# Kernel tuning notes

Hardware: AMD Instinct MI355X
Metric: run time of the kernel (lower is better)

## Reference

```python
import jax, jax.numpy as jnp
import numpy as np

EPS = 1e-12  # matches torch F.normalize eps


def _l2_normalize(x, axis=-1):
    # torch.F.normalize: x / max(||x||, eps)
    n = jnp.sqrt(jnp.sum(x * x, axis=axis, keepdims=True))
    return x / jnp.maximum(n, EPS)


def setup_inputs() -> dict:
    N, n_classes, embed_dim = 32768, 1000, 1024
    key = jax.random.key(0)
    k_feat, k_lab, k_proto = jax.random.split(key, 3)

    features = jax.random.normal(k_feat, (N, embed_dim), dtype=jnp.float32)

    # one-hot float labels, as expected by `torch.matmul(labels, self.mean_class)`
    y = jax.random.randint(k_lab, (N,), 0, n_classes)
    labels = jax.nn.one_hot(y, n_classes, dtype=jnp.float32)

    # predefined prototypes: orthonormal rows (ortho_group.rvs equivalent via QR)
    g = jax.random.normal(k_proto, (embed_dim, embed_dim), dtype=jnp.float32)
    q, _ = jnp.linalg.qr(g)
    mean_class = q[:n_classes]  # [n_classes, embed_dim], orthonormal rows

    return {"features": features, "labels": labels, "mean_class": mean_class}


def reference(features, labels, mean_class):
    # features: [N, D]; labels: [N, C] one-hot; mean_class: [C, D]
    # (3-D feature mean-pooling branch not exercised: inputs are 2-D)
    proto_y = labels @ mean_class                 # [N, D]
    f = _l2_normalize(features, axis=1)
    p = _l2_normalize(proto_y, axis=1)
    # diag(f @ p.T) == rowwise dot product -> same math, O(N*D) not O(N^2*D)
    cos = jnp.einsum("nd,nd->n", f, p)            # [N]
    return jnp.mean(1.0 - cos)
```

## Files before the change

kernel.cpp:

```cpp
#include <hip/hip_runtime.h>

constexpr int N_CLASSES = 1000;
constexpr int EMBED     = 1024;
constexpr int ROWS_PER_BLOCK = 8;

typedef float floatx4 __attribute__((ext_vector_type(4)));

__global__ __launch_bounds__(256) void angular_fused_kernel(
    const float* __restrict__ features,
    const float* __restrict__ labels,
    const float* __restrict__ mean_class,
    float* __restrict__ partials,
    int n_rows)
{
    const int tid  = threadIdx.x;
    const int lane = tid & 63;
    const int wave = tid >> 6;
    const int row0 = blockIdx.x * ROWS_PER_BLOCK;

    __shared__ int   s_cls[ROWS_PER_BLOCK];
    __shared__ float s_red[4];

    if (tid < N_CLASSES / 4) {
        #pragma unroll
        for (int r = 0; r < ROWS_PER_BLOCK; ++r) {
            const int row = row0 + r;
            if (row < n_rows) {
                const floatx4* lrow = (const floatx4*)(labels + (size_t)row * N_CLASSES);
                floatx4 v = __builtin_nontemporal_load(lrow + tid);
                if (v.x != 0.f || v.y != 0.f || v.z != 0.f || v.w != 0.f) {
                    int c = 4 * tid;
                    if      (v.y != 0.f) c += 1;
                    else if (v.z != 0.f) c += 2;
                    else if (v.w != 0.f) c += 3;
                    s_cls[r] = c;
                }
            }
        }
    }

    const int rA = row0 + 2 * wave;
    const int rB = rA + 1;
    const bool okA = rA < n_rows, okB = rB < n_rows;

    const floatx4* fArow = (const floatx4*)(features + (size_t)(okA ? rA : 0) * EMBED);
    const floatx4* fBrow = (const floatx4*)(features + (size_t)(okB ? rB : 0) * EMBED);
    floatx4 a0 = __builtin_nontemporal_load(fArow + lane);
    floatx4 a1 = __builtin_nontemporal_load(fArow + lane + 64);
    floatx4 a2 = __builtin_nontemporal_load(fArow + lane + 128);
    floatx4 a3 = __builtin_nontemporal_load(fArow + lane + 192);
    floatx4 b0 = __builtin_nontemporal_load(fBrow + lane);
    floatx4 b1 = __builtin_nontemporal_load(fBrow + lane + 64);
    floatx4 b2 = __builtin_nontemporal_load(fBrow + lane + 128);
    floatx4 b3 = __builtin_nontemporal_load(fBrow + lane + 192);

    __syncthreads();

    const int clsA = okA ? s_cls[2 * wave] : 0;
    const int clsB = okB ? s_cls[2 * wave + 1] : 0;
    const floatx4* pArow = (const floatx4*)(mean_class + (size_t)clsA * EMBED);
    const floatx4* pBrow = (const floatx4*)(mean_class + (size_t)clsB * EMBED);
    floatx4 pa0 = pArow[lane];
    floatx4 pa1 = pArow[lane + 64];
    floatx4 pa2 = pArow[lane + 128];
    floatx4 pa3 = pArow[lane + 192];
    floatx4 pb0 = pBrow[lane];
    floatx4 pb1 = pBrow[lane + 64];
    floatx4 pb2 = pBrow[lane + 128];
    floatx4 pb3 = pBrow[lane + 192];

    float ffA = 0.f, ppA = 0.f, fpA = 0.f;
    float ffB = 0.f, ppB = 0.f, fpB = 0.f;
    #define DOT3(FF, PP, FP, F, P) \
        FF += F.x*F.x + F.y*F.y + F.z*F.z + F.w*F.w; \
        PP += P.x*P.x + P.y*P.y + P.z*P.z + P.w*P.w; \
        FP += F.x*P.x + F.y*P.y + F.z*P.z + F.w*P.w;
    DOT3(ffA, ppA, fpA, a0, pa0) DOT3(ffA, ppA, fpA, a1, pa1)
    DOT3(ffA, ppA, fpA, a2, pa2) DOT3(ffA, ppA, fpA, a3, pa3)
    DOT3(ffB, ppB, fpB, b0, pb0) DOT3(ffB, ppB, fpB, b1, pb1)
    DOT3(ffB, ppB, fpB, b2, pb2) DOT3(ffB, ppB, fpB, b3, pb3)
    #undef DOT3

    #pragma unroll
    for (int msk = 1; msk < 64; msk <<= 1) {
        ffA += __shfl_xor(ffA, msk, 64);
        ppA += __shfl_xor(ppA, msk, 64);
        fpA += __shfl_xor(fpA, msk, 64);
        ffB += __shfl_xor(ffB, msk, 64);
        ppB += __shfl_xor(ppB, msk, 64);
        fpB += __shfl_xor(fpB, msk, 64);
    }

    float res = 0.f;
    if (okA) res += 1.0f - fpA / (fmaxf(sqrtf(ffA), 1e-12f) * fmaxf(sqrtf(ppA), 1e-12f));
    if (okB) res += 1.0f - fpB / (fmaxf(sqrtf(ffB), 1e-12f) * fmaxf(sqrtf(ppB), 1e-12f));

    if (lane == 0) s_red[wave] = res;
    __syncthreads();
    if (tid == 0)
        partials[blockIdx.x] = s_red[0] + s_red[1] + s_red[2] + s_red[3];
}

__global__ __launch_bounds__(256) void reduce_partials_kernel(
    const float* __restrict__ partials, int num_partials,
    float* __restrict__ out, float inv_n)
{
    const int tid  = threadIdx.x;
    const int lane = tid & 63;
    const int wave = tid >> 6;
    __shared__ float s_red[4];

    float acc = 0.0f;
    for (int i = tid; i < num_partials; i += 256)
        acc += partials[i];
    #pragma unroll
    for (int msk = 1; msk < 64; msk <<= 1)
        acc += __shfl_xor(acc, msk, 64);
    if (lane == 0) s_red[wave] = acc;
    __syncthreads();
    if (tid == 0)
        out[0] = (s_red[0] + s_red[1] + s_red[2] + s_red[3]) * inv_n;
}

extern "C" void kernel_launch(void* const* d_in, const int* in_sizes, int n_in,
                              void* d_out, int out_size, void* d_ws, size_t ws_size,
                              hipStream_t stream) {
    const float* features   = (const float*)d_in[0];
    const float* labels     = (const float*)d_in[1];
    const float* mean_class = (const float*)d_in[2];
    float* out = (float*)d_out;
    float* partials = (float*)d_ws;

    const int n_rows = in_sizes[0] / EMBED;
    const int num_blocks = (n_rows + ROWS_PER_BLOCK - 1) / ROWS_PER_BLOCK;

    angular_fused_kernel<<<num_blocks, 256, 0, stream>>>(
        features, labels, mean_class, partials, n_rows);
    reduce_partials_kernel<<<1, 256, 0, stream>>>(
        partials, num_blocks, out, 1.0f / (float)n_rows);
}
```

Measured before the change: 258.3 us.

## Stage one-hot label rows into LDS via async global_load_lds and scan per wave

Label rows are no longer scanned directly from global memory by 250 threads. Each wave now issues asynchronous global-to-LDS copies of its two label rows, and these overlap with the feature loads. After the barrier each wave scans its rows in LDS, then uses ballot and shuffle to pick the hot class index, made wave-uniform with readfirstlane. The nontemporal hints on the feature loads are also dropped. The aim is better memory-level parallelism on the dominant label traffic, at the cost of 32KB of LDS per block, which may reduce occupancy.

```diff
diff --git a/kernel.cpp b/kernel.cpp
--- a/kernel.cpp
+++ b/kernel.cpp
@@ -1,10 +1,19 @@
 #include <hip/hip_runtime.h>
+#include <stdint.h>
 
 constexpr int N_CLASSES = 1000;
 constexpr int EMBED     = 1024;
 constexpr int ROWS_PER_BLOCK = 8;
+constexpr int LAB_BYTES = N_CLASSES * 4;
 
 typedef float floatx4 __attribute__((ext_vector_type(4)));
+
+__device__ __forceinline__ void gl2lds16(const void* g, void* l) {
+    __builtin_amdgcn_global_load_lds(
+        (const __attribute__((address_space(1))) void*)g,
+        (__attribute__((address_space(3))) void*)l,
+        16, 0, 0);
+}
 
 __global__ __launch_bounds__(256) void angular_fused_kernel(
     const float* __restrict__ features,
@@ -18,46 +27,74 @@
     const int wave = tid >> 6;
     const int row0 = blockIdx.x * ROWS_PER_BLOCK;
 
-    __shared__ int   s_cls[ROWS_PER_BLOCK];
+    __shared__ __align__(16) char s_lab[ROWS_PER_BLOCK][LAB_BYTES];
     __shared__ float s_red[4];
-
-    if (tid < N_CLASSES / 4) {
-        #pragma unroll
-        for (int r = 0; r < ROWS_PER_BLOCK; ++r) {
-            const int row = row0 + r;
-            if (row < n_rows) {
-                const floatx4* lrow = (const floatx4*)(labels + (size_t)row * N_CLASSES);
-                floatx4 v = __builtin_nontemporal_load(lrow + tid);
-                if (v.x != 0.f || v.y != 0.f || v.z != 0.f || v.w != 0.f) {
-                    int c = 4 * tid;
-                    if      (v.y != 0.f) c += 1;
-                    else if (v.z != 0.f) c += 2;
-                    else if (v.w != 0.f) c += 3;
-                    s_cls[r] = c;
-                }
-            }
-        }
-    }
 
     const int rA = row0 + 2 * wave;
     const int rB = rA + 1;
     const bool okA = rA < n_rows, okB = rB < n_rows;
+    const int rAc = okA ? rA : 0;
+    const int rBc = okB ? rB : 0;
 
-    const floatx4* fArow = (const floatx4*)(features + (size_t)(okA ? rA : 0) * EMBED);
-    const floatx4* fBrow = (const floatx4*)(features + (size_t)(okB ? rB : 0) * EMBED);
-    floatx4 a0 = __builtin_nontemporal_load(fArow + lane);
-    floatx4 a1 = __builtin_nontemporal_load(fArow + lane + 64);
-    floatx4 a2 = __builtin_nontemporal_load(fArow + lane + 128);
-    floatx4 a3 = __builtin_nontemporal_load(fArow + lane + 192);
-    floatx4 b0 = __builtin_nontemporal_load(fBrow + lane);
-    floatx4 b1 = __builtin_nontemporal_load(fBrow + lane + 64);
-    floatx4 b2 = __builtin_nontemporal_load(fBrow + lane + 128);
-    floatx4 b3 = __builtin_nontemporal_load(fBrow + lane + 192);
+    {
+        const char* gA = (const char*)labels + (size_t)rAc * LAB_BYTES;
+        const char* gB = (const char*)labels + (size_t)rBc * LAB_BYTES;
+        char* lA = &s_lab[2 * wave][0];
+        char* lB = &s_lab[2 * wave + 1][0];
+        #pragma unroll
+        for (int c = 0; c < 3; ++c) {
+            gl2lds16(gA + c * 1024 + lane * 16, lA + c * 1024);
+            gl2lds16(gB + c * 1024 + lane * 16, lB + c * 1024);
+        }
+        if (lane < 58) {
+            gl2lds16(gA + 3072 + lane * 16, lA + 3072);
+            gl2lds16(gB + 3072 + lane * 16, lB + 3072);
+        }
+    }
+
+    const floatx4* fArow = (const floatx4*)(features + (size_t)rAc * EMBED);
+    const floatx4* fBrow = (const floatx4*)(features + (size_t)rBc * EMBED);
+    floatx4 a0 = fArow[lane];
+    floatx4 a1 = fArow[lane + 64];
+    floatx4 a2 = fArow[lane + 128];
+    floatx4 a3 = fArow[lane + 192];
+    floatx4 b0 = fBrow[lane];
+    floatx4 b1 = fBrow[lane + 64];
+    floatx4 b2 = fBrow[lane + 128];
+    floatx4 b3 = fBrow[lane + 192];
 
     __syncthreads();
 
-    const int clsA = okA ? s_cls[2 * wave] : 0;
-    const int clsB = okB ? s_cls[2 * wave + 1] : 0;
+    const floatx4* lAv = (const floatx4*)&s_lab[2 * wave][0];
+    const floatx4* lBv = (const floatx4*)&s_lab[2 * wave + 1][0];
+
+    int candA = -1, candB = -1;
+    #define SCAN(CAND, V, IDX) { \
+        floatx4 v_ = (V); int i_ = (IDX); \
+        if (v_.x != 0.f || v_.y != 0.f || v_.z != 0.f || v_.w != 0.f) { \
+            int c_ = 4 * i_; \
+            if      (v_.y != 0.f) c_ += 1; \
+            else if (v_.z != 0.f) c_ += 2; \
+            else if (v_.w != 0.f) c_ += 3; \
+            CAND = c_; \
+        } }
+    SCAN(candA, lAv[lane],        lane)
+    SCAN(candA, lAv[lane + 64],   lane + 64)
+    SCAN(candA, lAv[lane + 128],  lane + 128)
+    if (lane < 58) SCAN(candA, lAv[lane + 192], lane + 192)
+    SCAN(candB, lBv[lane],        lane)
+    SCAN(candB, lBv[lane + 64],   lane + 64)
+    SCAN(candB, lBv[lane + 128],  lane + 128)
+    if (lane < 58) SCAN(candB, lBv[lane + 192], lane + 192)
+    #undef SCAN
+
+    unsigned long long mA = __ballot(candA >= 0);
+    unsigned long long mB = __ballot(candB >= 0);
+    int clsA = __shfl(candA, __ffsll(mA) - 1, 64);
+    int clsB = __shfl(candB, __ffsll(mB) - 1, 64);
+    clsA = __builtin_amdgcn_readfirstlane(clsA);
+    clsB = __builtin_amdgcn_readfirstlane(clsB);
+
     const floatx4* pArow = (const floatx4*)(mean_class + (size_t)clsA * EMBED);
     const floatx4* pBrow = (const floatx4*)(mean_class + (size_t)clsB * EMBED);
     floatx4 pa0 = pArow[lane];
```

Result: slower. 280.8 us (+8.7%).
